# Kernel tuning notes

Measured on AMD Instinct MI355X. Metric: run time of the kernel, lower is better.

## Reference

```python
import jax, jax.numpy as jnp
import numpy as np

N = 50000
E = 1600000
X_DIM = 3
POS_DIM = 3
F_HID = 64
F_OUT = 64
G_HID = 64
G_OUT = 64


def _lin_init(key, fan_in, fan_out):
    kw, kb = jax.random.split(key)
    s = 1.0 / np.sqrt(fan_in)
    w = jax.random.uniform(kw, (fan_in, fan_out), minval=-s, maxval=s, dtype=jnp.float32)
    b = jax.random.uniform(kb, (fan_out,), minval=-s, maxval=s, dtype=jnp.float32)
    return w, b


def setup_inputs() -> dict:
    key = jax.random.key(0)
    ks = jax.random.split(key, 8)
    x = jax.random.normal(ks[0], (N, X_DIM), dtype=jnp.float32)
    pos = jax.random.normal(ks[1], (N, POS_DIM), dtype=jnp.float32)
    edge_index = jax.random.randint(ks[2], (2, E), 0, N, dtype=jnp.int64)
    f_w1, f_b1 = _lin_init(ks[3], X_DIM + POS_DIM, F_HID)
    f_w2, f_b2 = _lin_init(ks[4], F_HID, F_OUT)
    g_w1, g_b1 = _lin_init(ks[5], F_OUT + X_DIM, G_HID)
    g_w2, g_b2 = _lin_init(ks[6], G_HID, G_OUT)
    return {"x": x, "pos": pos, "edge_index": edge_index,
            "f_w1": f_w1, "f_b1": f_b1, "f_w2": f_w2, "f_b2": f_b2,
            "g_w1": g_w1, "g_b1": g_b1, "g_w2": g_w2, "g_b2": g_b2}


def reference(x, pos, edge_index, f_w1, f_b1, f_w2, f_b2, g_w1, g_b1, g_w2, g_b2):
    src = edge_index[0]  # j (source)
    dst = edge_index[1]  # i (target)
    # message: relu(f([x_j, pos_j - pos_i]))  (h(x_i) is dead code in the source)
    delta_pos = pos[src] - pos[dst]                      # [E, 3]
    m_in = jnp.concatenate([x[src], delta_pos], axis=1)  # [E, 6]
    h = jax.nn.celu(m_in @ f_w1 + f_b1)                  # [E, F_HID]
    msg = jax.nn.relu(h @ f_w2 + f_b2)                   # [E, F_OUT]
    # aggregate: scatter-max over target nodes; empty segments -> 0 (PyG behavior)
    aggr = jax.ops.segment_max(msg, dst, num_segments=N)
    aggr = jnp.where(jnp.isneginf(aggr), 0.0, aggr)      # [N, F_OUT]
    # update: g([aggr, x]) then final CELU (end_relu)
    u_in = jnp.concatenate([aggr, x], axis=1)            # [N, F_OUT + X_DIM]
    u = jax.nn.celu(u_in @ g_w1 + g_b1)
    out = u @ g_w2 + g_b2                                # [N, G_OUT]
    return jax.nn.celu(out)
```

## Files before the change

### kernel.cpp

```cpp
#include <hip/hip_runtime.h>
#include <hip/hip_fp16.h>
#include <math.h>

#define NN 50000
#define NE 1600000
#define NBKT 196
#define BKT_SHIFT 8
#define BCAP 16384

typedef unsigned int u32;
typedef unsigned long long u64;
typedef _Float16 f16x8 __attribute__((ext_vector_type(8)));
typedef _Float16 f16x4 __attribute__((ext_vector_type(4)));
typedef float f32x4 __attribute__((ext_vector_type(4)));

__device__ __forceinline__ float celu_fast(float v) {
    return v > 0.0f ? v : __expf(v) - 1.0f;
}

__device__ __forceinline__ __half* hptr(__half* base, int row, int c4) {
    return base + (row << 6) + ((c4 ^ ((row & 7) << 1)) << 2);
}

__global__ __launch_bounds__(256) void binA_prep_kernel(
    const int* __restrict__ ei, u32* __restrict__ gcur, u32* __restrict__ sd1,
    uint4* __restrict__ aggr4,
    const float* __restrict__ x, const float* __restrict__ pos,
    float* __restrict__ xp,
    const float* __restrict__ fw1, const float* __restrict__ fw2,
    const float* __restrict__ gw1, const float* __restrict__ gw2,
    __half* __restrict__ w1t, __half* __restrict__ w2t,
    __half* __restrict__ g1t, __half* __restrict__ g2t,
    float* __restrict__ w1x)
{
    const int tid = threadIdx.x;
    const int b = blockIdx.x;
    if (b == 391) {
        for (int i = tid; i < 4096; i += 256) {
            const int n = i >> 6, k = i & 63;
            w2t[i] = __float2half(fw2[k * 64 + n]);
            g1t[i] = __float2half(gw1[k * 64 + n]);
            g2t[i] = __float2half(gw2[k * 64 + n]);
        }
        for (int j = tid; j < 512; j += 256) {
            const int n = j >> 3, k = j & 7;
            w1t[j] = (k < 6) ? __float2half(fw1[k * 64 + n]) : __half(0.0f);
        }
        if (tid < 192) {
            const int c = tid >> 6, ch = tid & 63;
            w1x[tid] = gw1[(64 + c) * 64 + ch];
        }
        return;
    }

    for (int idx = b * 256 + tid; idx < NN * 64 / 4; idx += 391 * 256)
        aggr4[idx] = make_uint4(0u, 0u, 0u, 0u);
    {
        const int n = b * 256 + tid;
        if (n < NN) {
            float4 a, p;
            a.x = x[n * 3 + 0]; a.y = x[n * 3 + 1]; a.z = x[n * 3 + 2]; a.w = 0.f;
            p.x = pos[n * 3 + 0]; p.y = pos[n * 3 + 1]; p.z = pos[n * 3 + 2]; p.w = 0.f;
            *(float4*)&xp[n * 8 + 0] = a;
            *(float4*)&xp[n * 8 + 4] = p;
        }
    }

    __shared__ u32 s_hist[NBKT];
    __shared__ u32 s_res[NBKT];
    __shared__ u32 s_cur[NBKT];
    if (tid < NBKT) { s_hist[tid] = 0u; s_cur[tid] = 0u; }
    __syncthreads();

    const int e0 = b * 4096 + tid * 16;
    const bool valid = (e0 < NE);
    u32 ed[16];
    if (valid) {
        const int4* sp = (const int4*)&ei[e0];
        const int4* dp = (const int4*)&ei[NE + e0];
#pragma unroll
        for (int q = 0; q < 4; ++q) {
            int4 s4 = sp[q];
            int4 d4 = dp[q];
            ed[q * 4 + 0] = ((u32)d4.x << 16) | (u32)s4.x;
            ed[q * 4 + 1] = ((u32)d4.y << 16) | (u32)s4.y;
            ed[q * 4 + 2] = ((u32)d4.z << 16) | (u32)s4.z;
            ed[q * 4 + 3] = ((u32)d4.w << 16) | (u32)s4.w;
        }
#pragma unroll
        for (int q = 0; q < 16; ++q)
            atomicAdd(&s_hist[ed[q] >> 24], 1u);
    }
    __syncthreads();
    if (tid < NBKT && s_hist[tid]) s_res[tid] = atomicAdd(&gcur[tid], s_hist[tid]);
    __syncthreads();
    if (valid) {
#pragma unroll
        for (int q = 0; q < 16; ++q) {
            const u32 bb = ed[q] >> 24;
            const u32 r = atomicAdd(&s_cur[bb], 1u);
            const u32 p = s_res[bb] + r;
            if (p < BCAP) sd1[bb * BCAP + p] = ed[q];
        }
    }
}

__global__ __launch_bounds__(512) void sortB_kernel(const u32* __restrict__ sd1,
                                                    const u32* __restrict__ gcur,
                                                    u32* __restrict__ sd2) {
    __shared__ u32 s_scan[256];
    __shared__ u32 s_cnt[256];
    __shared__ u32 s_pos[256];
    const int tid = threadIdx.x;
    const int b = blockIdx.x;

    if (tid < 256) s_scan[tid] = (tid < NBKT) ? gcur[tid] : 0u;
    __syncthreads();
    for (int d = 1; d < 256; d <<= 1) {
        u32 t = 0u;
        if (tid < 256 && tid >= d) t = s_scan[tid - d];
        __syncthreads();
        if (tid < 256) s_scan[tid] += t;
        __syncthreads();
    }
    u32 cnt = gcur[b];
    if (cnt > BCAP) cnt = BCAP;
    const u32 outbase = s_scan[b] - cnt;
    const u32 src = (u32)b * BCAP;

    if (tid < 256) s_cnt[tid] = 0u;
    __syncthreads();
    for (u32 j = tid; j < cnt; j += 512)
        atomicAdd(&s_cnt[(sd1[src + j] >> 16) & 255u], 1u);
    __syncthreads();
    if (tid < 256) s_pos[tid] = s_cnt[tid];
    __syncthreads();
    for (int d = 1; d < 256; d <<= 1) {
        u32 t = 0u;
        if (tid < 256 && tid >= d) t = s_pos[tid - d];
        __syncthreads();
        if (tid < 256) s_pos[tid] += t;
        __syncthreads();
    }
    if (tid < 256) s_pos[tid] -= s_cnt[tid];
    __syncthreads();
    for (u32 j = tid; j < cnt; j += 512) {
        const u32 sd = sd1[src + j];
        const u32 dl = (sd >> 16) & 255u;
        const u32 r = atomicAdd(&s_pos[dl], 1u);
        sd2[outbase + r] = sd;
    }
}

__global__ __launch_bounds__(256, 4) void edge_fused_kernel(
    const float* __restrict__ xp,
    const u32* __restrict__ sdb,
    const __half* __restrict__ w1t, const float* __restrict__ fb1,
    const __half* __restrict__ w2t, const float* __restrict__ fb2,
    u32* __restrict__ aggr)
{
    __shared__ __align__(16) __half s_in[256 * 8];
    __shared__ __align__(16) __half s_h[256 * 64];
    __shared__ u32 s_d[256];
    __shared__ u32 s_start[257];
    __shared__ u32 s_nseg;

    const int tid = threadIdx.x;
    const int xcd = blockIdx.x & 7;
    const int idx = blockIdx.x >> 3;
    const int ebid = (xcd < 2) ? xcd * 782 + idx : 2 * 782 + (xcd - 2) * 781 + idx;

    const int i = ebid * 256 + tid;
    const u32 w = sdb[i];
    const int s = (int)(w & 0xFFFFu);
    const int d = (int)(w >> 16);
    s_d[tid] = (u32)d;

    {
        const float4* xp4 = (const float4*)xp;
        float4 axs = xp4[s * 2];
        float4 aps = xp4[s * 2 + 1];
        float4 apd = xp4[d * 2 + 1];
        union { uint4 u; __half2 h2[4]; } pk;
        pk.h2[0] = __floats2half2_rn(axs.x, axs.y);
        pk.h2[1] = __floats2half2_rn(axs.z, aps.x - apd.x);
        pk.h2[2] = __floats2half2_rn(aps.y - apd.y, aps.z - apd.z);
        pk.h2[3] = __floats2half2_rn(0.f, 0.f);
        *(uint4*)&s_in[tid * 8] = pk.u;
    }
    __syncthreads();

    const int l = tid & 63;
    const int wbase = tid & 192;
    const int lrow = l & 15;
    const int lhi = l >> 4;

    const f16x8 zero8 = {};
    f16x8 b1f[4];
#pragma unroll
    for (int nt = 0; nt < 4; ++nt) {
        b1f[nt] = zero8;
        if (lhi == 0)
            b1f[nt] = *(const f16x8*)&s_in[(wbase + nt * 16 + lrow) * 8];
    }

#pragma unroll
    for (int mt = 0; mt < 4; ++mt) {
        f16x8 a = zero8;
        if (lhi == 0) a = *(const f16x8*)&w1t[(mt * 16 + lrow) * 8];
        const f32x4 c0 = *(const f32x4*)&fb1[mt * 16 + lhi * 4];
#pragma unroll
        for (int nt = 0; nt < 4; ++nt) {
            f32x4 z = __builtin_amdgcn_mfma_f32_16x16x32_f16(a, b1f[nt], c0, 0, 0, 0);
            const int row = wbase + nt * 16 + lrow;
            union { uint2 u; __half2 h2[2]; } pk;
            pk.h2[0] = __floats2half2_rn(celu_fast(z[0]), celu_fast(z[1]));
            pk.h2[1] = __floats2half2_rn(celu_fast(z[2]), celu_fast(z[3]));
            *(uint2*)hptr(s_h, row, mt * 4 + lhi) = pk.u;
        }
    }

    if (tid < 64) {
        u32 base = 0;
        for (int c = 0; c < 4; ++c) {
            const int t = c * 64 + tid;
            const bool head = (t == 0) || (s_d[t] != s_d[t - 1]);
            const u64 m = __ballot(head);
            const u32 pos0 = base + (u32)__popcll(m & ((1ull << tid) - 1ull));
            if (head) s_start[pos0] = (u32)t;
            base += (u32)__popcll(m);
        }
        if (tid == 0) { s_nseg = base; s_start[base] = 256u; }
    }

    f16x8 afrag[4][2];
#pragma unroll
    for (int at = 0; at < 4; ++at)
#pragma unroll
        for (int kt = 0; kt < 2; ++kt)
            afrag[at][kt] = *(const f16x8*)(w2t + ((at * 16 + lrow) << 6) + kt * 32 + (lhi << 3));
    f32x4 bias2[4];
#pragma unroll
    for (int at = 0; at < 4; ++at)
        bias2[at] = *(const f32x4*)(fb2 + at * 16 + (lhi << 2));

    __syncthreads();

#pragma unroll
    for (int g = 0; g < 4; ++g) {
        const int rb = wbase + g * 16 + lrow;
        f32x4 acc[4];
#pragma unroll
        for (int at = 0; at < 4; ++at) acc[at] = bias2[at];
#pragma unroll
        for (int kt = 0; kt < 2; ++kt) {
            f16x8 b = *(const f16x8*)hptr(s_h, rb, (kt * 4 + lhi) * 2);
            acc[0] = __builtin_amdgcn_mfma_f32_16x16x32_f16(afrag[0][kt], b, acc[0], 0, 0, 0);
            acc[1] = __builtin_amdgcn_mfma_f32_16x16x32_f16(afrag[1][kt], b, acc[1], 0, 0, 0);
            acc[2] = __builtin_amdgcn_mfma_f32_16x16x32_f16(afrag[2][kt], b, acc[2], 0, 0, 0);
            acc[3] = __builtin_amdgcn_mfma_f32_16x16x32_f16(afrag[3][kt], b, acc[3], 0, 0, 0);
        }
#pragma unroll
        for (int at = 0; at < 4; ++at) {
            union { uint2 u; __half2 h2[2]; } pk;
            pk.h2[0] = __floats2half2_rn(acc[at][0], acc[at][1]);
            pk.h2[1] = __floats2half2_rn(acc[at][2], acc[at][3]);
            *(uint2*)hptr(s_h, rb, at * 4 + lhi) = pk.u;
        }
    }
    __syncthreads();

    const int hw = tid >> 5;
    const int lane2 = tid & 31;
    const int sub = lane2 >> 4;
    const int c8 = lane2 & 15;
    const u32 nseg = s_nseg;
    for (u32 j = (u32)hw; j < nseg; j += 8) {
        const u32 lo = s_start[j];
        const u32 hi = s_start[j + 1];
        const u32 node = s_d[lo];
        f16x4 m = {};
        for (u32 r0 = lo; r0 < hi; r0 += 2) {
            const u32 r = r0 + (u32)sub;
            if (r < hi) {
                f16x4 v = *(const f16x4*)hptr(s_h, (int)r, c8);
                m = __builtin_elementwise_max(m, v);
            }
        }
        union { f16x4 v; int w2[2]; } a, b;
        a.v = m;
        b.w2[0] = __shfl_down(a.w2[0], 16, 32);
        b.w2[1] = __shfl_down(a.w2[1], 16, 32);
        f16x4 mm = __builtin_elementwise_max(a.v, b.v);
        if (sub == 0) {
            if (lo > 0u && hi < 256u) {
                float4 st;
                st.x = fmaxf((float)mm[0], 0.f);
                st.y = fmaxf((float)mm[1], 0.f);
                st.z = fmaxf((float)mm[2], 0.f);
                st.w = fmaxf((float)mm[3], 0.f);
                *(float4*)((float*)aggr + (size_t)node * 64 + c8 * 4) = st;
            } else {
                u32* arow = aggr + (size_t)node * 64 + c8 * 4;
#pragma unroll
                for (int t = 0; t < 4; ++t) {
                    float f = (float)mm[t];
                    if (f > 0.f) atomicMax(&arow[t], __float_as_uint(f));
                }
            }
        }
    }
}

__global__ __launch_bounds__(256) void node_mfma_kernel(
    const float* __restrict__ xp,
    float* io,
    const __half* __restrict__ g1t, const float* __restrict__ w1x,
    const float* __restrict__ gb1,
    const __half* __restrict__ g2t, const float* __restrict__ gb2)
{
    __shared__ __align__(16) __half s_a[128 * 64];
    __shared__ __align__(16) __half s_u[128 * 64];
    __shared__ __align__(16) float s_x[128 * 4];

    const int tid = threadIdx.x;
    const int n0 = blockIdx.x * 128;

#pragma unroll
    for (int it = 0; it < 8; ++it) {
        const int idx = it * 256 + tid;
        const int row = idx >> 4, c8 = idx & 15;
        const int g = n0 + row;
        float4 v = make_float4(0.f, 0.f, 0.f, 0.f);
        if (g < NN) v = *(const float4*)&io[(size_t)g * 64 + c8 * 4];
        union { uint2 u; __half2 h2[2]; } pk;
        pk.h2[0] = __floats2half2_rn(v.x, v.y);
        pk.h2[1] = __floats2half2_rn(v.z, v.w);
        *(uint2*)hptr(s_a, row, c8) = pk.u;
    }
    if (tid < 128) {
        const int g = n0 + tid;
        float4 a = make_float4(0.f, 0.f, 0.f, 0.f);
        if (g < NN) a = *(const float4*)&xp[(size_t)g * 8];
        *(float4*)&s_x[tid * 4] = a;
    }
    __syncthreads();

    const int l = tid & 63;
    const int wv = tid >> 6;
    const int lrow = l & 15;
    const int lhi = l >> 4;

    f16x8 a1[4][2], a2[4][2];
    f32x4 bias1[4], bias2[4];
    f32x4 wx0[4], wx1[4], wx2[4];
#pragma unroll
    for (int at = 0; at < 4; ++at) {
#pragma unroll
        for (int kt = 0; kt < 2; ++kt) {
            const int off = ((at * 16 + lrow) << 6) + kt * 32 + (lhi << 3);
            a1[at][kt] = *(const f16x8*)(g1t + off);
            a2[at][kt] = *(const f16x8*)(g2t + off);
        }
        bias1[at] = *(const f32x4*)&gb1[at * 16 + lhi * 4];
        bias2[at] = *(const f32x4*)&gb2[at * 16 + lhi * 4];
        const int ch = at * 16 + lhi * 4;
        wx0[at] = *(const f32x4*)&w1x[0 * 64 + ch];
        wx1[at] = *(const f32x4*)&w1x[1 * 64 + ch];
        wx2[at] = *(const f32x4*)&w1x[2 * 64 + ch];
    }

#pragma unroll
    for (int g = 0; g < 2; ++g) {
        const int rb = wv * 32 + g * 16 + lrow;
        f32x4 acc[4];
#pragma unroll
        for (int at = 0; at < 4; ++at) acc[at] = bias1[at];
#pragma unroll
        for (int kt = 0; kt < 2; ++kt) {
            f16x8 b = *(const f16x8*)hptr(s_a, rb, (kt * 4 + lhi) * 2);
            acc[0] = __builtin_amdgcn_mfma_f32_16x16x32_f16(a1[0][kt], b, acc[0], 0, 0, 0);
            acc[1] = __builtin_amdgcn_mfma_f32_16x16x32_f16(a1[1][kt], b, acc[1], 0, 0, 0);
            acc[2] = __builtin_amdgcn_mfma_f32_16x16x32_f16(a1[2][kt], b, acc[2], 0, 0, 0);
            acc[3] = __builtin_amdgcn_mfma_f32_16x16x32_f16(a1[3][kt], b, acc[3], 0, 0, 0);
        }
        const float x0 = s_x[rb * 4 + 0];
        const float x1 = s_x[rb * 4 + 1];
        const float x2 = s_x[rb * 4 + 2];
#pragma unroll
        for (int at = 0; at < 4; ++at) {
            f32x4 z = acc[at];
#pragma unroll
            for (int t = 0; t < 4; ++t)
                z[t] = fmaf(x0, wx0[at][t], fmaf(x1, wx1[at][t], fmaf(x2, wx2[at][t], z[t])));
            union { uint2 u; __half2 h2[2]; } pk;
            pk.h2[0] = __floats2half2_rn(celu_fast(z[0]), celu_fast(z[1]));
            pk.h2[1] = __floats2half2_rn(celu_fast(z[2]), celu_fast(z[3]));
            *(uint2*)hptr(s_u, rb, at * 4 + lhi) = pk.u;
        }
    }
    __syncthreads();

#pragma unroll
    for (int g = 0; g < 2; ++g) {
        const int rb = wv * 32 + g * 16 + lrow;
        const int node = n0 + rb;
        f32x4 acc[4];
#pragma unroll
        for (int at = 0; at < 4; ++at) acc[at] = bias2[at];
#pragma unroll
        for (int kt = 0; kt < 2; ++kt) {
            f16x8 b = *(const f16x8*)hptr(s_u, rb, (kt * 4 + lhi) * 2);
            acc[0] = __builtin_amdgcn_mfma_f32_16x16x32_f16(a2[0][kt], b, acc[0], 0, 0, 0);
            acc[1] = __builtin_amdgcn_mfma_f32_16x16x32_f16(a2[1][kt], b, acc[1], 0, 0, 0);
            acc[2] = __builtin_amdgcn_mfma_f32_16x16x32_f16(a2[2][kt], b, acc[2], 0, 0, 0);
            acc[3] = __builtin_amdgcn_mfma_f32_16x16x32_f16(a2[3][kt], b, acc[3], 0, 0, 0);
        }
        if (node < NN) {
#pragma unroll
            for (int at = 0; at < 4; ++at) {
                float4 r;
                r.x = celu_fast(acc[at][0]);
                r.y = celu_fast(acc[at][1]);
                r.z = celu_fast(acc[at][2]);
                r.w = celu_fast(acc[at][3]);
                *(float4*)&io[(size_t)node * 64 + at * 16 + lhi * 4] = r;
            }
        }
    }
}


__global__ __launch_bounds__(256) void zero_kernel(float4* __restrict__ p, int n4) {
    int i = blockIdx.x * blockDim.x + threadIdx.x;
    if (i < n4) p[i] = make_float4(0.f, 0.f, 0.f, 0.f);
}

__global__ __launch_bounds__(256) void edge_atomic_kernel(
    const float* __restrict__ x, const float* __restrict__ pos,
    const int* __restrict__ ei,
    const float* __restrict__ fw1, const float* __restrict__ fb1,
    const float* __restrict__ fw2, const float* __restrict__ fb2,
    unsigned int* __restrict__ aggr)
{
    __shared__ __align__(16) float s_w1[6 * 64];
    __shared__ __align__(16) float s_b1[64];
    __shared__ __align__(16) float s_w2[64 * 64];
    __shared__ __align__(16) float s_b2[64];

    const int tid = threadIdx.x;
    for (int i = tid; i < 6 * 64; i += 256) s_w1[i] = fw1[i];
    for (int i = tid; i < 64 * 64; i += 256) s_w2[i] = fw2[i];
    if (tid < 64) { s_b1[tid] = fb1[tid]; s_b2[tid] = fb2[tid]; }
    __syncthreads();

    const int e = blockIdx.x * 256 + tid;
    if (e >= NE) return;

    const int s = ei[e];
    const int d = ei[NE + e];

    float in[6];
    in[0] = x[s * 3 + 0];
    in[1] = x[s * 3 + 1];
    in[2] = x[s * 3 + 2];
    in[3] = pos[s * 3 + 0] - pos[d * 3 + 0];
    in[4] = pos[s * 3 + 1] - pos[d * 3 + 1];
    in[5] = pos[s * 3 + 2] - pos[d * 3 + 2];

    float h[64];
#pragma unroll
    for (int k = 0; k < 64; k += 4) {
        float4 acc = *(const float4*)&s_b1[k];
#pragma unroll
        for (int q = 0; q < 6; ++q) {
            float4 w = *(const float4*)&s_w1[q * 64 + k];
            acc.x = fmaf(in[q], w.x, acc.x);
            acc.y = fmaf(in[q], w.y, acc.y);
            acc.z = fmaf(in[q], w.z, acc.z);
            acc.w = fmaf(in[q], w.w, acc.w);
        }
        h[k + 0] = celu_fast(acc.x);
        h[k + 1] = celu_fast(acc.y);
        h[k + 2] = celu_fast(acc.z);
        h[k + 3] = celu_fast(acc.w);
    }

    unsigned int* arow = aggr + (size_t)d * 64;
    for (int o = 0; o < 64; o += 4) {
        float4 acc = *(const float4*)&s_b2[o];
#pragma unroll
        for (int k = 0; k < 64; ++k) {
            float4 w = *(const float4*)&s_w2[k * 64 + o];
            acc.x = fmaf(h[k], w.x, acc.x);
            acc.y = fmaf(h[k], w.y, acc.y);
            acc.z = fmaf(h[k], w.z, acc.z);
            acc.w = fmaf(h[k], w.w, acc.w);
        }
        if (acc.x > 0.f) atomicMax(&arow[o + 0], __float_as_uint(acc.x));
        if (acc.y > 0.f) atomicMax(&arow[o + 1], __float_as_uint(acc.y));
        if (acc.z > 0.f) atomicMax(&arow[o + 2], __float_as_uint(acc.z));
        if (acc.w > 0.f) atomicMax(&arow[o + 3], __float_as_uint(acc.w));
    }
}

__global__ __launch_bounds__(256) void node_valu_kernel(
    const float* __restrict__ x,
    float* io,
    const float* __restrict__ gw1, const float* __restrict__ gb1,
    const float* __restrict__ gw2, const float* __restrict__ gb2)
{
    __shared__ __align__(16) float s_w1[67 * 64];
    __shared__ __align__(16) float s_b1[64];
    __shared__ __align__(16) float s_w2[64 * 64];
    __shared__ __align__(16) float s_b2[64];

    const int tid = threadIdx.x;
    for (int i = tid; i < 67 * 64; i += 256) s_w1[i] = gw1[i];
    for (int i = tid; i < 64 * 64; i += 256) s_w2[i] = gw2[i];
    if (tid < 64) { s_b1[tid] = gb1[tid]; s_b2[tid] = gb2[tid]; }
    __syncthreads();

    const int n = blockIdx.x * 256 + tid;
    if (n >= NN) return;

    float a[64];
#pragma unroll
    for (int k = 0; k < 64; k += 4) {
        float4 v = *(const float4*)&io[(size_t)n * 64 + k];
        a[k + 0] = v.x; a[k + 1] = v.y; a[k + 2] = v.z; a[k + 3] = v.w;
    }
    float xv[3];
    xv[0] = x[n * 3 + 0];
    xv[1] = x[n * 3 + 1];
    xv[2] = x[n * 3 + 2];

    float u[64];
    for (int j = 0; j < 64; j += 4) {
        float4 acc = *(const float4*)&s_b1[j];
#pragma unroll
        for (int k = 0; k < 64; ++k) {
            float4 w = *(const float4*)&s_w1[k * 64 + j];
            acc.x = fmaf(a[k], w.x, acc.x);
            acc.y = fmaf(a[k], w.y, acc.y);
            acc.z = fmaf(a[k], w.z, acc.z);
            acc.w = fmaf(a[k], w.w, acc.w);
        }
#pragma unroll
        for (int q = 0; q < 3; ++q) {
            float4 w = *(const float4*)&s_w1[(64 + q) * 64 + j];
            acc.x = fmaf(xv[q], w.x, acc.x);
            acc.y = fmaf(xv[q], w.y, acc.y);
            acc.z = fmaf(xv[q], w.z, acc.z);
            acc.w = fmaf(xv[q], w.w, acc.w);
        }
        u[j + 0] = celu_fast(acc.x);
        u[j + 1] = celu_fast(acc.y);
        u[j + 2] = celu_fast(acc.z);
        u[j + 3] = celu_fast(acc.w);
    }

    float* orow = &io[(size_t)n * 64];
    for (int j = 0; j < 64; j += 4) {
        float4 acc = *(const float4*)&s_b2[j];
#pragma unroll
        for (int k = 0; k < 64; ++k) {
            float4 w = *(const float4*)&s_w2[k * 64 + j];
            acc.x = fmaf(u[k], w.x, acc.x);
            acc.y = fmaf(u[k], w.y, acc.y);
            acc.z = fmaf(u[k], w.z, acc.z);
            acc.w = fmaf(u[k], w.w, acc.w);
        }
        float4 r;
        r.x = celu_fast(acc.x);
        r.y = celu_fast(acc.y);
        r.z = celu_fast(acc.z);
        r.w = celu_fast(acc.w);
        *(float4*)&orow[j] = r;
    }
}


extern "C" void kernel_launch(void* const* d_in, const int* in_sizes, int n_in,
                              void* d_out, int out_size, void* d_ws, size_t ws_size,
                              hipStream_t stream) {
    const float* x   = (const float*)d_in[0];
    const float* pos = (const float*)d_in[1];
    const int*   ei  = (const int*)d_in[2];
    const float* fw1 = (const float*)d_in[3];
    const float* fb1 = (const float*)d_in[4];
    const float* fw2 = (const float*)d_in[5];
    const float* fb2 = (const float*)d_in[6];
    const float* gw1 = (const float*)d_in[7];
    const float* gb1 = (const float*)d_in[8];
    const float* gw2 = (const float*)d_in[9];
    const float* gb2 = (const float*)d_in[10];
    float* out = (float*)d_out;

    const int n4 = NN * 64 / 4;
    const int NBE = (NE + 4095) / 4096;

    auto al = [](size_t v) { return (v + 255) & ~(size_t)255; };
    const size_t o_gcur = 0;
    const size_t o_w1t  = al(o_gcur + (size_t)NBKT * 4);
    const size_t o_w2t  = al(o_w1t + (size_t)64 * 8 * 2);
    const size_t o_g1t  = al(o_w2t + (size_t)64 * 64 * 2);
    const size_t o_g2t  = al(o_g1t + (size_t)64 * 64 * 2);
    const size_t o_w1x  = al(o_g2t + (size_t)64 * 64 * 2);
    const size_t o_xp   = al(o_w1x + (size_t)192 * 4);
    const size_t o_sd1  = al(o_xp + (size_t)NN * 8 * 4);
    const size_t o_sd2  = al(o_sd1 + (size_t)NBKT * BCAP * 4);
    const size_t need   = o_sd2 + (size_t)NE * 4;

    if (ws_size >= need) {
        char* w = (char*)d_ws;
        u32*    gcur = (u32*)(w + o_gcur);
        __half* w1t  = (__half*)(w + o_w1t);
        __half* w2t  = (__half*)(w + o_w2t);
        __half* g1t  = (__half*)(w + o_g1t);
        __half* g2t  = (__half*)(w + o_g2t);
        float*  w1x  = (float*)(w + o_w1x);
        float*  xp   = (float*)(w + o_xp);
        u32*    sd1  = (u32*)(w + o_sd1);
        u32*    sd2  = (u32*)(w + o_sd2);

        (void)hipMemsetAsync(gcur, 0, (size_t)NBKT * 4, stream);
        binA_prep_kernel<<<NBE + 1, 256, 0, stream>>>(ei, gcur, sd1, (uint4*)out,
                                                      x, pos, xp,
                                                      fw1, fw2, gw1, gw2,
                                                      w1t, w2t, g1t, g2t, w1x);
        sortB_kernel<<<NBKT, 512, 0, stream>>>(sd1, gcur, sd2);
        edge_fused_kernel<<<NE / 256, 256, 0, stream>>>(xp, sd2, w1t, fb1,
                                                        w2t, fb2, (u32*)out);
        node_mfma_kernel<<<(NN + 127) / 128, 256, 0, stream>>>(xp, out, g1t, w1x,
                                                               gb1, g2t, gb2);
    } else {
        zero_kernel<<<(n4 + 255) / 256, 256, 0, stream>>>((float4*)out, n4);
        edge_atomic_kernel<<<NE / 256, 256, 0, stream>>>(x, pos, ei, fw1, fb1,
                                                         fw2, fb2, (unsigned int*)out);
        node_valu_kernel<<<(NN + 255) / 256, 256, 0, stream>>>(x, out, gw1, gb1,
                                                               gw2, gb2);
    }
}
```

Before: 123.3 us.

## Stage bucketed edges in LDS before global scatter in binning and sort kernels

The binning kernel now runs 197 blocks of 512 threads, each handling 8192 edges. It first scatters edges locally into an LDS staging buffer ordered by bucket, then writes each bucket's run to global memory contiguously, one wavefront per bucket. The sort kernel likewise scatters into an LDS stage and then writes the sorted bucket out coalesced, falling back to direct global scatter when a bucket exceeds the stage capacity. Both changes aim to replace random scattered global writes with coalesced ones, at the cost of extra LDS use (32KB and 48KB), extra scan passes and syncs, and fewer blocks in the binning kernel.

New measurement: 115.9 us, median of 3. 6.0% less time.

```diff
diff --git a/kernel.cpp b/kernel.cpp
--- a/kernel.cpp
+++ b/kernel.cpp
@@ -7,6 +7,7 @@
 #define NBKT 196
 #define BKT_SHIFT 8
 #define BCAP 16384
+#define SCAP 12288
 
 typedef unsigned int u32;
 typedef unsigned long long u64;
@@ -22,7 +23,7 @@
     return base + (row << 6) + ((c4 ^ ((row & 7) << 1)) << 2);
 }
 
-__global__ __launch_bounds__(256) void binA_prep_kernel(
+__global__ __launch_bounds__(512) void binA_prep_kernel(
     const int* __restrict__ ei, u32* __restrict__ gcur, u32* __restrict__ sd1,
     uint4* __restrict__ aggr4,
     const float* __restrict__ x, const float* __restrict__ pos,
@@ -35,16 +36,16 @@
 {
     const int tid = threadIdx.x;
     const int b = blockIdx.x;
-    if (b == 391) {
-        for (int i = tid; i < 4096; i += 256) {
+    if (b == 196) {
+        for (int i = tid; i < 4096; i += 512) {
             const int n = i >> 6, k = i & 63;
             w2t[i] = __float2half(fw2[k * 64 + n]);
             g1t[i] = __float2half(gw1[k * 64 + n]);
             g2t[i] = __float2half(gw2[k * 64 + n]);
         }
-        for (int j = tid; j < 512; j += 256) {
-            const int n = j >> 3, k = j & 7;
-            w1t[j] = (k < 6) ? __float2half(fw1[k * 64 + n]) : __half(0.0f);
+        if (tid < 512) {
+            const int n = tid >> 3, k = tid & 7;
+            w1t[tid] = (k < 6) ? __float2half(fw1[k * 64 + n]) : __half(0.0f);
         }
         if (tid < 192) {
             const int c = tid >> 6, ch = tid & 63;
@@ -53,10 +54,10 @@
         return;
     }
 
-    for (int idx = b * 256 + tid; idx < NN * 64 / 4; idx += 391 * 256)
+    for (int idx = b * 512 + tid; idx < NN * 64 / 4; idx += 196 * 512)
         aggr4[idx] = make_uint4(0u, 0u, 0u, 0u);
     {
-        const int n = b * 256 + tid;
+        const int n = b * 512 + tid;
         if (n < NN) {
             float4 a, p;
             a.x = x[n * 3 + 0]; a.y = x[n * 3 + 1]; a.z = x[n * 3 + 2]; a.w = 0.f;
@@ -68,11 +69,15 @@
 
     __shared__ u32 s_hist[NBKT];
     __shared__ u32 s_res[NBKT];
+    __shared__ u32 s_lofs[NBKT];
     __shared__ u32 s_cur[NBKT];
+    __shared__ u32 s_scan[256];
+    __shared__ u32 s_stage[8192];
+
     if (tid < NBKT) { s_hist[tid] = 0u; s_cur[tid] = 0u; }
     __syncthreads();
 
-    const int e0 = b * 4096 + tid * 16;
+    const int e0 = b * 8192 + tid * 16;
     const bool valid = (e0 < NE);
     u32 ed[16];
     if (valid) {
@@ -93,14 +98,36 @@
     }
     __syncthreads();
     if (tid < NBKT && s_hist[tid]) s_res[tid] = atomicAdd(&gcur[tid], s_hist[tid]);
+    if (tid < 256) s_scan[tid] = (tid < NBKT) ? s_hist[tid] : 0u;
+    __syncthreads();
+    for (int d = 1; d < 256; d <<= 1) {
+        u32 t = 0u;
+        if (tid < 256 && tid >= d) t = s_scan[tid - d];
+        __syncthreads();
+        if (tid < 256) s_scan[tid] += t;
+        __syncthreads();
+    }
+    if (tid < NBKT) s_lofs[tid] = s_scan[tid] - s_hist[tid];
     __syncthreads();
     if (valid) {
 #pragma unroll
         for (int q = 0; q < 16; ++q) {
             const u32 bb = ed[q] >> 24;
             const u32 r = atomicAdd(&s_cur[bb], 1u);
-            const u32 p = s_res[bb] + r;
-            if (p < BCAP) sd1[bb * BCAP + p] = ed[q];
+            s_stage[s_lofs[bb] + r] = ed[q];
+        }
+    }
+    __syncthreads();
+    const int wv = tid >> 6;
+    const int lane = tid & 63;
+    for (int bk = wv; bk < NBKT; bk += 8) {
+        const u32 cnt = s_hist[bk];
+        if (!cnt) continue;
+        const u32 lo = s_lofs[bk];
+        const u32 gres = s_res[bk];
+        for (u32 j = (u32)lane; j < cnt; j += 64) {
+            const u32 p = gres + j;
+            if (p < BCAP) sd1[(u32)bk * BCAP + p] = s_stage[lo + j];
         }
     }
 }
@@ -111,6 +138,7 @@
     __shared__ u32 s_scan[256];
     __shared__ u32 s_cnt[256];
     __shared__ u32 s_pos[256];
+    __shared__ u32 s_stage[SCAP];
     const int tid = threadIdx.x;
     const int b = blockIdx.x;
 
@@ -144,11 +172,24 @@
     }
     if (tid < 256) s_pos[tid] -= s_cnt[tid];
     __syncthreads();
-    for (u32 j = tid; j < cnt; j += 512) {
-        const u32 sd = sd1[src + j];
-        const u32 dl = (sd >> 16) & 255u;
-        const u32 r = atomicAdd(&s_pos[dl], 1u);
-        sd2[outbase + r] = sd;
+
+    if (cnt <= SCAP) {
+        for (u32 j = tid; j < cnt; j += 512) {
+            const u32 sd = sd1[src + j];
+            const u32 dl = (sd >> 16) & 255u;
+            const u32 r = atomicAdd(&s_pos[dl], 1u);
+            s_stage[r] = sd;
+        }
+        __syncthreads();
+        for (u32 j = tid; j < cnt; j += 512)
+            sd2[outbase + j] = s_stage[j];
+    } else {
+        for (u32 j = tid; j < cnt; j += 512) {
+            const u32 sd = sd1[src + j];
+            const u32 dl = (sd >> 16) & 255u;
+            const u32 r = atomicAdd(&s_pos[dl], 1u);
+            sd2[outbase + r] = sd;
+        }
     }
 }
 
@@ -598,7 +639,6 @@
     float* out = (float*)d_out;
 
     const int n4 = NN * 64 / 4;
-    const int NBE = (NE + 4095) / 4096;
 
     auto al = [](size_t v) { return (v + 255) & ~(size_t)255; };
     const size_t o_gcur = 0;
@@ -625,10 +665,10 @@
         u32*    sd2  = (u32*)(w + o_sd2);
 
         (void)hipMemsetAsync(gcur, 0, (size_t)NBKT * 4, stream);
-        binA_prep_kernel<<<NBE + 1, 256, 0, stream>>>(ei, gcur, sd1, (uint4*)out,
-                                                      x, pos, xp,
-                                                      fw1, fw2, gw1, gw2,
-                                                      w1t, w2t, g1t, g2t, w1x);
+        binA_prep_kernel<<<197, 512, 0, stream>>>(ei, gcur, sd1, (uint4*)out,
+                                                  x, pos, xp,
+                                                  fw1, fw2, gw1, gw2,
+                                                  w1t, w2t, g1t, g2t, w1x);
         sortB_kernel<<<NBKT, 512, 0, stream>>>(sd1, gcur, sd2);
         edge_fused_kernel<<<NE / 256, 256, 0, stream>>>(xp, sd2, w1t, fb1,
                                                         w2t, fb2, (u32*)out);
```
